# Kernel optimization log

Measured on AMD Instinct MI355X. Metric: run time of the kernel, lower is better.

Reference implementation:

```python
import jax, jax.numpy as jnp
import numpy as np

B, N, C, E, O = 4, 128, 256, 128, 128
NEG = -1.0e9


def setup_inputs() -> dict:
    key = jax.random.key(0)
    ks = jax.random.split(key, 24)
    s = jnp.float32(0.02)
    w = lambda k, shp: jax.random.normal(k, shp, jnp.float32) * s
    mm = jax.random.randint(ks[3], (B, N, N), 0, 2).astype(bool)
    return {
        "z": jax.random.normal(ks[0], (B, N, C), jnp.float32),
        "e": jax.random.normal(ks[1], (B, N, N, E), jnp.float32),
        "g": jax.random.normal(ks[2], (B, C // 2), jnp.float32),
        "mask": jnp.ones((B, N), bool),
        "msgs_mask": mm | jnp.eye(N, dtype=bool)[None],  # ensure each max-col nonempty
        "Wt1": w(ks[4], (C, 8)), "Wt2": w(ks[5], (C, 8)), "Wt3": w(ks[6], (C, 8)),
        "Wte1": w(ks[7], (E, 8)), "Wte2": w(ks[8], (E, 8)), "Wte3": w(ks[9], (E, 8)),
        "Wtg": w(ks[10], (C // 2, 8)),
        "Wm1": w(ks[11], (C, O)), "Wm2": w(ks[12], (C, O)),
        "Wme": w(ks[13], (E, O)), "Wmg": w(ks[14], (C // 2, O)),
        "Wmlp1": w(ks[15], (O, O)), "Wmlp2": w(ks[16], (O, O)),
        "WU1": w(ks[17], (C, O)), "WU2": w(ks[18], (O, O)), "WU3": w(ks[19], (8, O)),
    }


def reference(z, e, g, mask, msgs_mask, Wt1, Wt2, Wt3, Wte1, Wte2, Wte3, Wtg,
              Wm1, Wm2, Wme, Wmg, Wmlp1, Wmlp2, WU1, WU2, WU3):
    m = mask[..., None]  # (B,N,1)
    # --- triplet path ---
    t1 = jnp.where(m, z @ Wt1, 0.0)  # (B,N,8)
    t2 = jnp.where(m, z @ Wt2, 0.0)
    t3 = jnp.where(m, z @ Wt3, 0.0)
    te1 = e @ Wte1  # (B,N,N,8)
    te2 = e @ Wte2
    te3 = e @ Wte3
    tg = g @ Wtg  # (B,8)
    # (B,N,N,N,8) 7-way broadcast sum
    tri = (t1[:, :, None, None, :] + t2[:, None, :, None, :] + t3[:, None, None, :, :]
           + te1[:, :, :, None, :] + te2[:, :, None, :, :] + te3[:, None, :, :, :]
           + tg[:, None, None, None, :])
    msk_tri = mask[:, None, None, :] | mask[:, None, :, None] | mask[:, :, None, None]
    tri = jnp.where(msk_tri[..., None], tri, NEG)
    tri_msgs = jnp.max(tri, axis=1) @ WU3  # (B,N,N,O)
    # --- pairwise message path ---
    m1 = jnp.where(m, z @ Wm1, 0.0)  # (B,N,O)
    m2 = jnp.where(m, z @ Wm2, 0.0)
    me = jnp.where(msgs_mask[..., None], e @ Wme, 0.0)  # (B,N,N,O)
    mg = g @ Wmg  # (B,O)
    msgs = m1[:, None, :, :] + m2[:, :, None, :] + me + mg[:, None, None, :]
    msgs = jax.nn.relu(msgs) @ Wmlp1  # num_layers=2 MLP: (ReLU,Lin)x2
    msgs = jax.nn.relu(msgs) @ Wmlp2
    msgs = jnp.where(msgs_mask[..., None], msgs, NEG)
    msgs = jnp.max(msgs, axis=1)  # (B,N,O)
    ret = z @ WU1 + msgs @ WU2
    return (ret, msgs, tri_msgs)
```

## Files before the change

kernel.cpp:

```cpp
#include <hip/hip_runtime.h>
#include <hip/hip_bf16.h>
#include <cstdint>
#include <cstddef>

namespace {

constexpr int B = 4, N = 128, C = 256, E = 128, O = 128, CH = 8;
constexpr float NEGV = -1.0e9f;

constexpr size_t SZ_TE_F  = (size_t)B * N * N * CH / 2;
constexpr size_t OFF_TE1T = 0;
constexpr size_t OFF_TE2  = OFF_TE1T + SZ_TE_F;
constexpr size_t OFF_TE3  = OFF_TE2 + SZ_TE_F;
constexpr size_t OFF_M1   = OFF_TE3 + SZ_TE_F;
constexpr size_t OFF_M2   = OFF_M1 + (size_t)B * N * O;
constexpr size_t OFF_ZU1  = OFF_M2 + (size_t)B * N * O;
constexpr size_t OFF_T1   = OFF_ZU1 + (size_t)B * N * O;
constexpr size_t OFF_T2   = OFF_T1 + (size_t)B * N * CH;
constexpr size_t OFF_T3   = OFF_T2 + (size_t)B * N * CH;
constexpr size_t OFF_TG   = OFF_T3 + (size_t)B * N * CH;
constexpr size_t OFF_WT   = OFF_TG + (size_t)B * CH;
constexpr size_t OFF_PART = OFF_WT + (size_t)3 * O * E / 2;

typedef __attribute__((ext_vector_type(4))) float f32x4;
typedef __attribute__((ext_vector_type(8))) short bf16x8;
typedef __attribute__((ext_vector_type(8))) unsigned short u16x8;

__device__ __forceinline__ unsigned short f2b(float f) {
  unsigned u = __float_as_uint(f);
  u = (u + 0x7fffu + ((u >> 16) & 1u)) >> 16;
  return (unsigned short)u;
}
__device__ __forceinline__ float b2f(unsigned short u) {
  return __uint_as_float((unsigned)u << 16);
}

}

__global__ __launch_bounds__(256) void k_prep(
    const float* __restrict__ z, const float* __restrict__ g,
    const float* __restrict__ e,
    const float* __restrict__ Wt1, const float* __restrict__ Wt2,
    const float* __restrict__ Wt3, const float* __restrict__ Wtg,
    const float* __restrict__ Wm1, const float* __restrict__ Wm2,
    const float* __restrict__ Wmg, const float* __restrict__ WU1,
    const float* __restrict__ Wte1, const float* __restrict__ Wte2,
    const float* __restrict__ Wte3,
    const float* __restrict__ Wme, const float* __restrict__ Wmlp1,
    const float* __restrict__ Wmlp2, float* __restrict__ ws) {
  __shared__ __align__(16) char smem[25600];
  const int blk = blockIdx.x;
  const int t = threadIdx.x;

  if (blk < 512) {
    unsigned short* wpack = (unsigned short*)(smem);
    unsigned short* ebuf  = (unsigned short*)(smem + 8704);
    unsigned short* outl  = (unsigned short*)(smem + 17408);
    unsigned short* te1T = (unsigned short*)(ws + OFF_TE1T);
    unsigned short* te2  = (unsigned short*)(ws + OFF_TE2);
    unsigned short* te3  = (unsigned short*)(ws + OFF_TE3);
    const int b = blk >> 7, i = blk & 127;

    for (int x = t; x < 3072; x += 256) {
      const int m = x >> 10, rem = x & 1023, k = rem >> 3, c = rem & 7;
      const float* W = (m == 0) ? Wte1 : ((m == 1) ? Wte2 : Wte3);
      const int row = m * 8 + c;
      wpack[row * 136 + k] = f2b(W[rem]);
    }
    for (int x = t; x < 1024; x += 256) {
      const int row = 24 + (x >> 7), col = x & 127;
      wpack[row * 136 + col] = 0;
    }

    const float* erow = e + ((size_t)(b * N) + i) * N * E;
    const int lane = t & 63, wid = t >> 6;
    const int li = lane & 15, lk8 = (lane >> 4) * 8, lq4 = (lane >> 4) * 4;
    const int jt = wid & 1, ct = wid >> 1;

    for (int j0 = 0; j0 < N; j0 += 32) {
      __syncthreads();
      for (int x = t; x < 1024; x += 256) {
        const int r = x >> 5, seg = x & 31;
        const float4 v = *reinterpret_cast<const float4*>(
            &erow[(size_t)(j0 + r) * E + seg * 4]);
        ushort4 pk;
        pk.x = f2b(v.x); pk.y = f2b(v.y); pk.z = f2b(v.z); pk.w = f2b(v.w);
        *reinterpret_cast<ushort4*>(&ebuf[r * 136 + seg * 4]) = pk;
      }
      __syncthreads();
      f32x4 acc = {0.f, 0.f, 0.f, 0.f};
#pragma unroll
      for (int kt = 0; kt < 4; ++kt) {
        const int rw = ct * 16 + li, ra = jt * 16 + li;
        const bf16x8 wf = *reinterpret_cast<const bf16x8*>(
            &wpack[rw * 136 + kt * 32 + lk8]);
        const bf16x8 af = *reinterpret_cast<const bf16x8*>(
            &ebuf[ra * 136 + kt * 32 + lk8]);
        acc = __builtin_amdgcn_mfma_f32_16x16x32_bf16(wf, af, acc, 0, 0, 0);
      }
      const int c0 = ct * 16 + lq4;
      if (c0 < 24) {
        ushort4 pk;
        pk.x = f2b(acc[0]); pk.y = f2b(acc[1]);
        pk.z = f2b(acc[2]); pk.w = f2b(acc[3]);
        *reinterpret_cast<ushort4*>(&outl[(j0 + jt * 16 + li) * 32 + c0]) = pk;
      }
    }
    __syncthreads();
    for (int x = t; x < 384; x += 256) {
      const int m = x >> 7, j = x & 127;
      const u16x8 v = *reinterpret_cast<const u16x8*>(&outl[j * 32 + m * 8]);
      if (m == 0)
        *reinterpret_cast<u16x8*>(&te1T[(((size_t)(b * N) + j) * N + i) * CH]) = v;
      else if (m == 1)
        *reinterpret_cast<u16x8*>(&te2[(((size_t)(b * N) + i) * N + j) * CH]) = v;
      else
        *reinterpret_cast<u16x8*>(&te3[(((size_t)(b * N) + i) * N + j) * CH]) = v;
    }
  } else if (blk < 1024) {
    float* zrow = (float*)(smem);
    float* grow = (float*)(smem + 1024);
    const int bn = blk - 512;
    const int b = bn >> 7, n = bn & 127;

    for (int k = t; k < C; k += 256) zrow[k] = z[((size_t)(b * N) + n) * C + k];
    if (t < C / 2) grow[t] = g[(size_t)b * (C / 2) + t];
    __syncthreads();

    {
      const int o = t & 127;
      const float* W = (t < 128) ? Wm1 : Wm2;
      float acc = 0.f;
#pragma unroll 8
      for (int k = 0; k < C; ++k) acc += zrow[k] * W[(size_t)k * O + o];
      if (t < 128) {
        float mgacc = 0.f;
        for (int k = 0; k < C / 2; ++k) mgacc += grow[k] * Wmg[(size_t)k * O + o];
        acc += mgacc;
        ws[OFF_M1 + ((size_t)(b * N) + n) * O + o] = acc;
      } else {
        ws[OFF_M2 + ((size_t)(b * N) + n) * O + o] = acc;
      }
    }
    if (t < 128) {
      float acc = 0.f;
#pragma unroll 8
      for (int k = 0; k < C; ++k) acc += zrow[k] * WU1[(size_t)k * O + t];
      ws[OFF_ZU1 + ((size_t)(b * N) + n) * O + t] = acc;
    } else if (t < 152) {
      const int idx = t - 128;
      const int which = idx >> 3, c = idx & 7;
      const float* W = (which == 0) ? Wt1 : ((which == 1) ? Wt2 : Wt3);
      float acc = 0.f;
      for (int k = 0; k < C; ++k) acc += zrow[k] * W[(size_t)k * CH + c];
      const size_t off = (which == 0) ? OFF_T1 : ((which == 1) ? OFF_T2 : OFF_T3);
      ws[off + ((size_t)(b * N) + n) * CH + c] = acc;
    }
    if (n == 0 && t >= 152 && t < 160) {
      const int c = t - 152;
      float acc = 0.f;
      for (int k = 0; k < C / 2; ++k) acc += grow[k] * Wtg[(size_t)k * CH + c];
      ws[OFF_TG + (size_t)b * CH + c] = acc;
    }
  } else {
    const int which = blk - 1024;
    const float* W = (which == 0) ? Wme : ((which == 1) ? Wmlp1 : Wmlp2);
    unsigned short* dst = (unsigned short*)(ws + OFF_WT) + (size_t)which * O * E;
    for (int x = t; x < O * E; x += 256) {
      const int o = x >> 7, k = x & 127;
      dst[x] = f2b(W[(size_t)k * O + o]);
    }
  }
}

__global__ __launch_bounds__(512) void k_main(
    const float* __restrict__ e, const void* __restrict__ msk,
    const float* __restrict__ WU3, const float* __restrict__ ws_c,
    float* __restrict__ ws, float* __restrict__ out_tri) {
  __shared__ __align__(16) char smem[33856];
  const int blk = blockIdx.x;
  const int t = threadIdx.x;

  if (blk < 256) {
    unsigned short* act0 = (unsigned short*)(smem);
    unsigned short* act1 = (unsigned short*)(smem + 8704);
    float* m2s = (float*)(smem + 17408);
    int* fmtp = (int*)(smem + 33792);
    const int jg = blk & 15, ig = (blk >> 4) & 3, b = blk >> 6;
    const int j0 = jg * 8, i0g = ig * 32;
    constexpr int LDK = 136;

    const int lane = t & 63, wid = t >> 6;
    const int li = lane & 15;
    const int lk8 = (lane >> 4) * 8;
    const int lq4 = (lane >> 4) * 4;

    if (t < 64) {
      const unsigned w = ((const unsigned*)msk)[t];
      const float f = __uint_as_float(w);
      const unsigned long long bad_int = __ballot(w > 1u);
      const unsigned long long bad_flt = __ballot(!(f == 0.f || f == 1.f));
      if (t == 0) *fmtp = (bad_int == 0ull) ? 0 : ((bad_flt == 0ull) ? 2 : 1);
    }

    const unsigned short* wts = (const unsigned short*)(ws_c + OFF_WT);
    bf16x8 wf0[4], wf1[4], wf2[4];
#pragma unroll
    for (int kt = 0; kt < 4; ++kt) {
      const size_t off = (size_t)(wid * 16 + li) * E + kt * 32 + lk8;
      wf0[kt] = *reinterpret_cast<const bf16x8*>(&wts[off]);
      wf1[kt] = *reinterpret_cast<const bf16x8*>(&wts[(size_t)O * E + off]);
      wf2[kt] = *reinterpret_cast<const bf16x8*>(&wts[(size_t)2 * O * E + off]);
    }
    for (int x = t; x < 32 * O; x += 512)
      m2s[x] = ws_c[OFF_M2 + ((size_t)(b * N) + i0g + (x >> 7)) * O + (x & 127)];
    __syncthreads();
    const int fmt = *fmtp;

    const int iA = i0g + li, iB = i0g + 16 + li;
    const int srow = t >> 3, sseg = t & 7;

    float4 ev;
    if (t < 256)
      ev = *reinterpret_cast<const float4*>(
          &e[(((size_t)(b * N) + i0g + srow) * N + j0) * E + sseg * 4]);
    float4 m1c = *reinterpret_cast<const float4*>(
        &ws_c[OFF_M1 + ((size_t)(b * N) + j0) * O + wid * 16 + lq4]);
    int mkAc, mkBc;
    {
      const size_t ia = ((size_t)(b * N) + iA) * N + j0;
      const size_t ib = ((size_t)(b * N) + iB) * N + j0;
      if (fmt == 0) { mkAc = ((const int*)msk)[ia] != 0; mkBc = ((const int*)msk)[ib] != 0; }
      else if (fmt == 1) { mkAc = ((const unsigned char*)msk)[ia] != 0; mkBc = ((const unsigned char*)msk)[ib] != 0; }
      else { mkAc = ((const float*)msk)[ia] != 0.f; mkBc = ((const float*)msk)[ib] != 0.f; }
    }
    if (t < 256) {
      ushort4 pk;
      pk.x = f2b(ev.x); pk.y = f2b(ev.y); pk.z = f2b(ev.z); pk.w = f2b(ev.w);
      *reinterpret_cast<ushort4*>(&act0[srow * LDK + sseg * 4]) = pk;
    }
    __syncthreads();

    unsigned short* actc = act0;
    unsigned short* actn = act1;
    const int o0 = wid * 16 + lq4;

    for (int jj = 0; jj < 8; ++jj) {
      const int j = j0 + jj;
      const int jn = (jj < 7) ? j + 1 : j;

      bf16x8 af[2][4];
      f32x4 acc[2];

#pragma unroll
      for (int it = 0; it < 2; ++it)
#pragma unroll
        for (int kt = 0; kt < 4; ++kt)
          af[it][kt] = *reinterpret_cast<const bf16x8*>(
              &actc[(it * 16 + li) * LDK + kt * 32 + lk8]);
      if (t < 256)
        ev = *reinterpret_cast<const float4*>(
            &e[(((size_t)(b * N) + i0g + srow) * N + jn) * E + sseg * 4]);
      float4 m1n = *reinterpret_cast<const float4*>(
          &ws_c[OFF_M1 + ((size_t)(b * N) + jn) * O + o0]);
      int mkAn, mkBn;
      {
        const size_t ia = ((size_t)(b * N) + iA) * N + jn;
        const size_t ib = ((size_t)(b * N) + iB) * N + jn;
        if (fmt == 0) { mkAn = ((const int*)msk)[ia] != 0; mkBn = ((const int*)msk)[ib] != 0; }
        else if (fmt == 1) { mkAn = ((const unsigned char*)msk)[ia] != 0; mkBn = ((const unsigned char*)msk)[ib] != 0; }
        else { mkAn = ((const float*)msk)[ia] != 0.f; mkBn = ((const float*)msk)[ib] != 0.f; }
      }
      acc[0] = (f32x4){0.f, 0.f, 0.f, 0.f};
      acc[1] = (f32x4){0.f, 0.f, 0.f, 0.f};
#pragma unroll
      for (int kt = 0; kt < 4; ++kt) {
        acc[0] = __builtin_amdgcn_mfma_f32_16x16x32_bf16(wf0[kt], af[0][kt], acc[0], 0, 0, 0);
        acc[1] = __builtin_amdgcn_mfma_f32_16x16x32_bf16(wf0[kt], af[1][kt], acc[1], 0, 0, 0);
      }
      __syncthreads();
#pragma unroll
      for (int it = 0; it < 2; ++it) {
        const int i = it * 16 + li;
        const float mk = (it ? mkBc : mkAc) ? 1.f : 0.f;
        const float4 m2v = *reinterpret_cast<const float4*>(&m2s[i * O + o0]);
        ushort4 pk;
        pk.x = f2b(fmaxf(acc[it][0] * mk + m2v.x + m1c.x, 0.f));
        pk.y = f2b(fmaxf(acc[it][1] * mk + m2v.y + m1c.y, 0.f));
        pk.z = f2b(fmaxf(acc[it][2] * mk + m2v.z + m1c.z, 0.f));
        pk.w = f2b(fmaxf(acc[it][3] * mk + m2v.w + m1c.w, 0.f));
        *reinterpret_cast<ushort4*>(&actc[i * LDK + o0]) = pk;
      }
      __syncthreads();

#pragma unroll
      for (int it = 0; it < 2; ++it)
#pragma unroll
        for (int kt = 0; kt < 4; ++kt)
          af[it][kt] = *reinterpret_cast<const bf16x8*>(
              &actc[(it * 16 + li) * LDK + kt * 32 + lk8]);
      acc[0] = (f32x4){0.f, 0.f, 0.f, 0.f};
      acc[1] = (f32x4){0.f, 0.f, 0.f, 0.f};
#pragma unroll
      for (int kt = 0; kt < 4; ++kt) {
        acc[0] = __builtin_amdgcn_mfma_f32_16x16x32_bf16(wf1[kt], af[0][kt], acc[0], 0, 0, 0);
        acc[1] = __builtin_amdgcn_mfma_f32_16x16x32_bf16(wf1[kt], af[1][kt], acc[1], 0, 0, 0);
      }
      __syncthreads();
#pragma unroll
      for (int it = 0; it < 2; ++it) {
        const int i = it * 16 + li;
        ushort4 pk;
        pk.x = f2b(fmaxf(acc[it][0], 0.f));
        pk.y = f2b(fmaxf(acc[it][1], 0.f));
        pk.z = f2b(fmaxf(acc[it][2], 0.f));
        pk.w = f2b(fmaxf(acc[it][3], 0.f));
        *reinterpret_cast<ushort4*>(&actc[i * LDK + o0]) = pk;
      }
      __syncthreads();

#pragma unroll
      for (int it = 0; it < 2; ++it)
#pragma unroll
        for (int kt = 0; kt < 4; ++kt)
          af[it][kt] = *reinterpret_cast<const bf16x8*>(
              &actc[(it * 16 + li) * LDK + kt * 32 + lk8]);
      acc[0] = (f32x4){0.f, 0.f, 0.f, 0.f};
      acc[1] = (f32x4){0.f, 0.f, 0.f, 0.f};
#pragma unroll
      for (int kt = 0; kt < 4; ++kt) {
        acc[0] = __builtin_amdgcn_mfma_f32_16x16x32_bf16(wf2[kt], af[0][kt], acc[0], 0, 0, 0);
        acc[1] = __builtin_amdgcn_mfma_f32_16x16x32_bf16(wf2[kt], af[1][kt], acc[1], 0, 0, 0);
      }
      if (t < 256) {
        ushort4 pk;
        pk.x = f2b(ev.x); pk.y = f2b(ev.y); pk.z = f2b(ev.z); pk.w = f2b(ev.w);
        *reinterpret_cast<ushort4*>(&actn[srow * LDK + sseg * 4]) = pk;
      }
      {
        float v0 = fmaxf(mkAc ? acc[0][0] : NEGV, mkBc ? acc[1][0] : NEGV);
        float v1 = fmaxf(mkAc ? acc[0][1] : NEGV, mkBc ? acc[1][1] : NEGV);
        float v2 = fmaxf(mkAc ? acc[0][2] : NEGV, mkBc ? acc[1][2] : NEGV);
        float v3 = fmaxf(mkAc ? acc[0][3] : NEGV, mkBc ? acc[1][3] : NEGV);
#pragma unroll
        for (int off = 1; off < 16; off <<= 1) {
          v0 = fmaxf(v0, __shfl_xor(v0, off));
          v1 = fmaxf(v1, __shfl_xor(v1, off));
          v2 = fmaxf(v2, __shfl_xor(v2, off));
          v3 = fmaxf(v3, __shfl_xor(v3, off));
        }
        if (li == 0) {
          float* part = ws + OFF_PART + (((size_t)(b * N) + j) * 4 + ig) * O;
          *reinterpret_cast<float4*>(&part[o0]) = make_float4(v0, v1, v2, v3);
        }
      }
      __syncthreads();
      unsigned short* tmp = actc; actc = actn; actn = tmp;
      m1c = m1n; mkAc = mkAn; mkBc = mkBn;
    }
  } else {
    float* A4   = (float*)(smem);
    float* wu3  = (float*)(smem + 16384);
    float* trif = (float*)(smem + 20480);
    float* t2j4 = (float*)(smem + 28672);
    float* tgb  = (float*)(smem + 28800);
    const int blk2 = blk - 256;
    const int kh = blk2 & 1, jt = (blk2 >> 1) & 31, b = blk2 >> 6;
    const int j0 = jt * 4;

    const unsigned short* te1T = (const unsigned short*)(ws_c + OFF_TE1T);
    const unsigned short* te2p =
        (const unsigned short*)(ws_c + OFF_TE2) + (size_t)b * N * N * CH;
    const unsigned short* te3p = (const unsigned short*)(ws_c + OFF_TE3);
    const float* t1p = ws_c + OFF_T1 + (size_t)b * N * CH;
    const float* t3p = ws_c + OFF_T3 + (size_t)b * N * CH;

    {
      const int idx8 = t * 8;
      const int jj = idx8 >> 10, i = (idx8 & 1023) >> 3;
      const u16x8 tv = *reinterpret_cast<const u16x8*>(
          &te1T[((size_t)(b * N) + j0 + jj) * N * CH + i * 8]);
      const float4 t1a = *reinterpret_cast<const float4*>(&t1p[i * 8]);
      const float4 t1b = *reinterpret_cast<const float4*>(&t1p[i * 8 + 4]);
      float4 av0, av1;
      av0.x = b2f(tv[0]) + t1a.x; av0.y = b2f(tv[1]) + t1a.y;
      av0.z = b2f(tv[2]) + t1a.z; av0.w = b2f(tv[3]) + t1a.w;
      av1.x = b2f(tv[4]) + t1b.x; av1.y = b2f(tv[5]) + t1b.y;
      av1.z = b2f(tv[6]) + t1b.z; av1.w = b2f(tv[7]) + t1b.w;
      *reinterpret_cast<float4*>(&A4[idx8]) = av0;
      *reinterpret_cast<float4*>(&A4[idx8 + 4]) = av1;
    }
    if (t < 256)
      *reinterpret_cast<float4*>(&wu3[t * 4]) =
          *reinterpret_cast<const float4*>(&WU3[t * 4]);
    if (t < 32)
      t2j4[t] = ws_c[OFF_T2 + ((size_t)(b * N) + j0 + (t >> 3)) * CH + (t & 7)];
    if (t < 8) tgb[t] = ws_c[OFF_TG + (size_t)b * CH + t];
    __syncthreads();

    const int io = t & 7, kl = t >> 3;
    const int kg = kh * 64 + kl;
    const size_t kbase = (size_t)kg * CH;
    float core[4][8];
#pragma unroll
    for (int jj = 0; jj < 4; ++jj)
#pragma unroll
      for (int c = 0; c < 8; ++c) core[jj][c] = -3.0e38f;

#pragma unroll 2
    for (int i0 = 0; i0 < N; i0 += 8) {
      const int i = i0 + io;
      const u16x8 rv =
          *reinterpret_cast<const u16x8*>(&te2p[(size_t)i * N * CH + kbase]);
      float r[8];
#pragma unroll
      for (int c = 0; c < 8; ++c) r[c] = b2f(rv[c]);
#pragma unroll
      for (int jj = 0; jj < 4; ++jj) {
        const float4 a0 = *reinterpret_cast<const float4*>(&A4[jj * 1024 + i * 8]);
        const float4 a1 = *reinterpret_cast<const float4*>(&A4[jj * 1024 + i * 8 + 4]);
        core[jj][0] = fmaxf(core[jj][0], a0.x + r[0]);
        core[jj][1] = fmaxf(core[jj][1], a0.y + r[1]);
        core[jj][2] = fmaxf(core[jj][2], a0.z + r[2]);
        core[jj][3] = fmaxf(core[jj][3], a0.w + r[3]);
        core[jj][4] = fmaxf(core[jj][4], a1.x + r[4]);
        core[jj][5] = fmaxf(core[jj][5], a1.y + r[5]);
        core[jj][6] = fmaxf(core[jj][6], a1.z + r[6]);
        core[jj][7] = fmaxf(core[jj][7], a1.w + r[7]);
      }
    }
#pragma unroll
    for (int jj = 0; jj < 4; ++jj)
#pragma unroll
      for (int c = 0; c < 8; ++c) {
        core[jj][c] = fmaxf(core[jj][c], __shfl_xor(core[jj][c], 1));
        core[jj][c] = fmaxf(core[jj][c], __shfl_xor(core[jj][c], 2));
        core[jj][c] = fmaxf(core[jj][c], __shfl_xor(core[jj][c], 4));
      }
#pragma unroll
    for (int jj = 0; jj < 4; ++jj) {
      float cv = core[jj][0];
#pragma unroll
      for (int c = 1; c < 8; ++c) cv = (io == c) ? core[jj][c] : cv;
      const unsigned short t3e =
          te3p[((size_t)(b * N) + j0 + jj) * N * CH + kbase + io];
      trif[jj * 512 + kl * 8 + io] =
          cv + t2j4[jj * 8 + io] + t3p[kbase + io] + b2f(t3e) + tgb[io];
    }
    __syncthreads();

    const int o = t & 127, rh = t >> 7;
    float wcol[8];
#pragma unroll
    for (int c = 0; c < 8; ++c) wcol[c] = wu3[c * 128 + o];
#pragma unroll 4
    for (int q = 0; q < 64; ++q) {
      const int row = q * 4 + rh;
      const int jj = row >> 6, klr = row & 63;
      const float4 f0 = *reinterpret_cast<const float4*>(&trif[row * 8]);
      const float4 f1 = *reinterpret_cast<const float4*>(&trif[row * 8 + 4]);
      float acc2 = f0.x * wcol[0] + f0.y * wcol[1] + f0.z * wcol[2] +
                   f0.w * wcol[3] + f1.x * wcol[4] + f1.y * wcol[5] +
                   f1.z * wcol[6] + f1.w * wcol[7];
      out_tri[((size_t)(b * N) + j0 + jj) * N * O +
              (size_t)(kh * 64 + klr) * O + o] = acc2;
    }
  }
}

__global__ __launch_bounds__(256) void k_fin(
    const float* __restrict__ WU2, const float* __restrict__ ws,
    float* __restrict__ out_ret, float* __restrict__ out_msgs) {
  const int blk = blockIdx.x;
  const int b = blk >> 7, j = blk & 127;
  const int t = threadIdx.x;
  __shared__ float msgsrow[O];
  __shared__ float red[2][O];

  const float* part = ws + OFF_PART + ((size_t)(b * N) + j) * 4 * O;
  if (t < O) {
    const float m = fmaxf(fmaxf(part[t], part[O + t]),
                          fmaxf(part[2 * O + t], part[3 * O + t]));
    msgsrow[t] = m;
    out_msgs[((size_t)(b * N) + j) * O + t] = m;
  }
  __syncthreads();

  const int o = t & 127, h = t >> 7;
  float acc = 0.f;
#pragma unroll 8
  for (int p = h * 64; p < h * 64 + 64; ++p)
    acc += msgsrow[p] * WU2[(size_t)p * O + o];
  red[h][o] = acc;
  __syncthreads();
  if (t < O) {
    out_ret[((size_t)(b * N) + j) * O + t] =
        ws[OFF_ZU1 + ((size_t)(b * N) + j) * O + t] + red[0][t] + red[1][t];
  }
}

extern "C" void kernel_launch(void* const* d_in, const int* in_sizes, int n_in,
                              void* d_out, int out_size, void* d_ws,
                              size_t ws_size, hipStream_t stream) {
  const float* z    = (const float*)d_in[0];
  const float* e    = (const float*)d_in[1];
  const float* g    = (const float*)d_in[2];
  const void*  mmsk = d_in[4];
  const float* Wt1  = (const float*)d_in[5];
  const float* Wt2  = (const float*)d_in[6];
  const float* Wt3  = (const float*)d_in[7];
  const float* Wte1 = (const float*)d_in[8];
  const float* Wte2 = (const float*)d_in[9];
  const float* Wte3 = (const float*)d_in[10];
  const float* Wtg  = (const float*)d_in[11];
  const float* Wm1  = (const float*)d_in[12];
  const float* Wm2  = (const float*)d_in[13];
  const float* Wme  = (const float*)d_in[14];
  const float* Wmg  = (const float*)d_in[15];
  const float* Wmlp1= (const float*)d_in[16];
  const float* Wmlp2= (const float*)d_in[17];
  const float* WU1  = (const float*)d_in[18];
  const float* WU2  = (const float*)d_in[19];
  const float* WU3  = (const float*)d_in[20];

  float* ws = (float*)d_ws;
  float* out_ret  = (float*)d_out;
  float* out_msgs = out_ret + (size_t)B * N * O;
  float* out_tri  = out_msgs + (size_t)B * N * O;

  k_prep<<<1027, dim3(256), 0, stream>>>(z, g, e, Wt1, Wt2, Wt3, Wtg, Wm1, Wm2,
                                         Wmg, WU1, Wte1, Wte2, Wte3, Wme, Wmlp1,
                                         Wmlp2, ws);
  k_main<<<512, dim3(512), 0, stream>>>(e, mmsk, WU3, ws, ws, out_tri);
  k_fin<<<B * N, dim3(256), 0, stream>>>(WU2, ws, out_ret, out_msgs);
}
```

Measured before the change: 63.96 us.

## Load e directly into MFMA operand registers in prep; widen e prefetch in message kernel

```diff
diff --git a/kernel.cpp b/kernel.cpp
--- a/kernel.cpp
+++ b/kernel.cpp
@@ -34,6 +34,11 @@
 __device__ __forceinline__ float b2f(unsigned short u) {
   return __uint_as_float((unsigned)u << 16);
 }
+__device__ __forceinline__ ushort4 f2b4(float4 v) {
+  ushort4 pk;
+  pk.x = f2b(v.x); pk.y = f2b(v.y); pk.z = f2b(v.z); pk.w = f2b(v.w);
+  return pk;
+}
 
 }
 
@@ -48,14 +53,13 @@
     const float* __restrict__ Wte3,
     const float* __restrict__ Wme, const float* __restrict__ Wmlp1,
     const float* __restrict__ Wmlp2, float* __restrict__ ws) {
-  __shared__ __align__(16) char smem[25600];
+  __shared__ __align__(16) char smem[17408];
   const int blk = blockIdx.x;
   const int t = threadIdx.x;
 
   if (blk < 512) {
     unsigned short* wpack = (unsigned short*)(smem);
-    unsigned short* ebuf  = (unsigned short*)(smem + 8704);
-    unsigned short* outl  = (unsigned short*)(smem + 17408);
+    unsigned short* outl  = (unsigned short*)(smem + 8704);
     unsigned short* te1T = (unsigned short*)(ws + OFF_TE1T);
     unsigned short* te2  = (unsigned short*)(ws + OFF_TE2);
     unsigned short* te3  = (unsigned short*)(ws + OFF_TE3);
@@ -71,39 +75,47 @@
       const int row = 24 + (x >> 7), col = x & 127;
       wpack[row * 136 + col] = 0;
     }
+    __syncthreads();
 
     const float* erow = e + ((size_t)(b * N) + i) * N * E;
     const int lane = t & 63, wid = t >> 6;
     const int li = lane & 15, lk8 = (lane >> 4) * 8, lq4 = (lane >> 4) * 4;
     const int jt = wid & 1, ct = wid >> 1;
-
-    for (int j0 = 0; j0 < N; j0 += 32) {
-      __syncthreads();
-      for (int x = t; x < 1024; x += 256) {
-        const int r = x >> 5, seg = x & 31;
-        const float4 v = *reinterpret_cast<const float4*>(
-            &erow[(size_t)(j0 + r) * E + seg * 4]);
-        ushort4 pk;
-        pk.x = f2b(v.x); pk.y = f2b(v.y); pk.z = f2b(v.z); pk.w = f2b(v.w);
-        *reinterpret_cast<ushort4*>(&ebuf[r * 136 + seg * 4]) = pk;
-      }
-      __syncthreads();
+    const int c0 = ct * 16 + lq4;
+
+    bf16x8 wf[4];
+#pragma unroll
+    for (int kt = 0; kt < 4; ++kt) {
+      const int rw = ct * 16 + li;
+      wf[kt] = *reinterpret_cast<const bf16x8*>(&wpack[rw * 136 + kt * 32 + lk8]);
+    }
+
+#pragma unroll 2
+    for (int step = 0; step < 4; ++step) {
+      const int jrow = step * 32 + jt * 16 + li;
+      const float* er = erow + (size_t)jrow * E;
+      float4 v[4][2];
+#pragma unroll
+      for (int kt = 0; kt < 4; ++kt) {
+        v[kt][0] = *reinterpret_cast<const float4*>(&er[kt * 32 + lk8]);
+        v[kt][1] = *reinterpret_cast<const float4*>(&er[kt * 32 + lk8 + 4]);
+      }
       f32x4 acc = {0.f, 0.f, 0.f, 0.f};
 #pragma unroll
       for (int kt = 0; kt < 4; ++kt) {
-        const int rw = ct * 16 + li, ra = jt * 16 + li;
-        const bf16x8 wf = *reinterpret_cast<const bf16x8*>(
-            &wpack[rw * 136 + kt * 32 + lk8]);
-        const bf16x8 af = *reinterpret_cast<const bf16x8*>(
-            &ebuf[ra * 136 + kt * 32 + lk8]);
-        acc = __builtin_amdgcn_mfma_f32_16x16x32_bf16(wf, af, acc, 0, 0, 0);
-      }
-      const int c0 = ct * 16 + lq4;
+        u16x8 af;
+        af[0] = f2b(v[kt][0].x); af[1] = f2b(v[kt][0].y);
+        af[2] = f2b(v[kt][0].z); af[3] = f2b(v[kt][0].w);
+        af[4] = f2b(v[kt][1].x); af[5] = f2b(v[kt][1].y);
+        af[6] = f2b(v[kt][1].z); af[7] = f2b(v[kt][1].w);
+        acc = __builtin_amdgcn_mfma_f32_16x16x32_bf16(
+            wf[kt], (bf16x8)af, acc, 0, 0, 0);
+      }
       if (c0 < 24) {
         ushort4 pk;
         pk.x = f2b(acc[0]); pk.y = f2b(acc[1]);
         pk.z = f2b(acc[2]); pk.w = f2b(acc[3]);
-        *reinterpret_cast<ushort4*>(&outl[(j0 + jt * 16 + li) * 32 + c0]) = pk;
+        *reinterpret_cast<ushort4*>(&outl[jrow * 32 + c0]) = pk;
       }
     }
     __syncthreads();
@@ -131,10 +143,11 @@
       const int o = t & 127;
       const float* W = (t < 128) ? Wm1 : Wm2;
       float acc = 0.f;
-#pragma unroll 8
+#pragma unroll 16
       for (int k = 0; k < C; ++k) acc += zrow[k] * W[(size_t)k * O + o];
       if (t < 128) {
         float mgacc = 0.f;
+#pragma unroll 8
         for (int k = 0; k < C / 2; ++k) mgacc += grow[k] * Wmg[(size_t)k * O + o];
         acc += mgacc;
         ws[OFF_M1 + ((size_t)(b * N) + n) * O + o] = acc;
@@ -144,7 +157,7 @@
     }
     if (t < 128) {
       float acc = 0.f;
-#pragma unroll 8
+#pragma unroll 16
       for (int k = 0; k < C; ++k) acc += zrow[k] * WU1[(size_t)k * O + t];
       ws[OFF_ZU1 + ((size_t)(b * N) + n) * O + t] = acc;
     } else if (t < 152) {
@@ -152,6 +165,7 @@
       const int which = idx >> 3, c = idx & 7;
       const float* W = (which == 0) ? Wt1 : ((which == 1) ? Wt2 : Wt3);
       float acc = 0.f;
+#pragma unroll 8
       for (int k = 0; k < C; ++k) acc += zrow[k] * W[(size_t)k * CH + c];
       const size_t off = (which == 0) ? OFF_T1 : ((which == 1) ? OFF_T2 : OFF_T3);
       ws[off + ((size_t)(b * N) + n) * CH + c] = acc;
@@ -218,12 +232,15 @@
     const int fmt = *fmtp;
 
     const int iA = i0g + li, iB = i0g + 16 + li;
-    const int srow = t >> 3, sseg = t & 7;
-
-    float4 ev;
-    if (t < 256)
-      ev = *reinterpret_cast<const float4*>(
-          &e[(((size_t)(b * N) + i0g + srow) * N + j0) * E + sseg * 4]);
+    const int prow0 = t >> 5;
+    const int prow1 = 16 + (t >> 5);
+    const int pseg = t & 31;
+
+    float4 ev0, ev1;
+    ev0 = *reinterpret_cast<const float4*>(
+        &e[(((size_t)(b * N) + i0g + prow0) * N + j0) * E + pseg * 4]);
+    ev1 = *reinterpret_cast<const float4*>(
+        &e[(((size_t)(b * N) + i0g + prow1) * N + j0) * E + pseg * 4]);
     float4 m1c = *reinterpret_cast<const float4*>(
         &ws_c[OFF_M1 + ((size_t)(b * N) + j0) * O + wid * 16 + lq4]);
     int mkAc, mkBc;
@@ -234,11 +251,8 @@
       else if (fmt == 1) { mkAc = ((const unsigned char*)msk)[ia] != 0; mkBc = ((const unsigned char*)msk)[ib] != 0; }
       else { mkAc = ((const float*)msk)[ia] != 0.f; mkBc = ((const float*)msk)[ib] != 0.f; }
     }
-    if (t < 256) {
-      ushort4 pk;
-      pk.x = f2b(ev.x); pk.y = f2b(ev.y); pk.z = f2b(ev.z); pk.w = f2b(ev.w);
-      *reinterpret_cast<ushort4*>(&act0[srow * LDK + sseg * 4]) = pk;
-    }
+    *reinterpret_cast<ushort4*>(&act0[prow0 * LDK + pseg * 4]) = f2b4(ev0);
+    *reinterpret_cast<ushort4*>(&act0[prow1 * LDK + pseg * 4]) = f2b4(ev1);
     __syncthreads();
 
     unsigned short* actc = act0;
@@ -258,9 +272,10 @@
         for (int kt = 0; kt < 4; ++kt)
           af[it][kt] = *reinterpret_cast<const bf16x8*>(
               &actc[(it * 16 + li) * LDK + kt * 32 + lk8]);
-      if (t < 256)
-        ev = *reinterpret_cast<const float4*>(
-            &e[(((size_t)(b * N) + i0g + srow) * N + jn) * E + sseg * 4]);
+      ev0 = *reinterpret_cast<const float4*>(
+          &e[(((size_t)(b * N) + i0g + prow0) * N + jn) * E + pseg * 4]);
+      ev1 = *reinterpret_cast<const float4*>(
+          &e[(((size_t)(b * N) + i0g + prow1) * N + jn) * E + pseg * 4]);
       float4 m1n = *reinterpret_cast<const float4*>(
           &ws_c[OFF_M1 + ((size_t)(b * N) + jn) * O + o0]);
       int mkAn, mkBn;
@@ -332,11 +347,8 @@
         acc[0] = __builtin_amdgcn_mfma_f32_16x16x32_bf16(wf2[kt], af[0][kt], acc[0], 0, 0, 0);
         acc[1] = __builtin_amdgcn_mfma_f32_16x16x32_bf16(wf2[kt], af[1][kt], acc[1], 0, 0, 0);
       }
-      if (t < 256) {
-        ushort4 pk;
-        pk.x = f2b(ev.x); pk.y = f2b(ev.y); pk.z = f2b(ev.z); pk.w = f2b(ev.w);
-        *reinterpret_cast<ushort4*>(&actn[srow * LDK + sseg * 4]) = pk;
-      }
+      *reinterpret_cast<ushort4*>(&actn[prow0 * LDK + pseg * 4]) = f2b4(ev0);
+      *reinterpret_cast<ushort4*>(&actn[prow1 * LDK + pseg * 4]) = f2b4(ev1);
       {
         float v0 = fmaxf(mkAc ? acc[0][0] : NEGV, mkBc ? acc[1][0] : NEGV);
         float v1 = fmaxf(mkAc ? acc[0][1] : NEGV, mkBc ? acc[1][1] : NEGV);
```

New measurement: 79.81 us. +24.8%, slower.
